# Optimization experiments

Hardware: AMD Instinct MI355X
Metric: run time of the kernel (lower is better)

Reference implementation:

```python
import jax, jax.numpy as jnp
import numpy as np

N, E, F = 50000, 800000, 16  # nodes, edges, per-quaternion-component features


def setup_inputs() -> dict:
    key = jax.random.key(0)
    ks = jax.random.split(key, 6)
    q = jax.random.normal(ks[0], (4, N, F), jnp.float32)          # node quaternion feats (r,i,j,k)
    edge_attr = jax.random.normal(ks[1], (4, E, F), jnp.float32)  # edge quaternion feats
    edge_index = jax.random.randint(ks[2], (2, E), 0, N)          # [src; dst]
    W1 = jax.random.normal(ks[3], (4, F, F), jnp.float32) * 0.1   # QLinear 1 weights (r,i,j,k)
    b1 = jnp.zeros((4, F), jnp.float32)
    W2 = jax.random.normal(ks[4], (4, F, F), jnp.float32) * 0.1   # QLinear 2 weights
    b2 = jnp.zeros((4, F), jnp.float32)
    beta = jnp.ones((1,), jnp.float32)                            # softmax temperature
    return {"q": q, "edge_attr": edge_attr, "edge_index": edge_index,
            "W1": W1, "b1": b1, "W2": W2, "b2": b2, "beta": beta}


def _qlinear(x, W, b):
    # Quaternion (Hamilton) linear: x [4,M,F_in], W [4,F_in,F_out], b [4,F_out]
    xr, xi, xj, xk = x
    Wr, Wi, Wj, Wk = W
    r = xr @ Wr - xi @ Wi - xj @ Wj - xk @ Wk
    i = xr @ Wi + xi @ Wr + xj @ Wk - xk @ Wj
    j = xr @ Wj - xi @ Wk + xj @ Wr + xk @ Wi
    k = xr @ Wk + xi @ Wj - xj @ Wi + xk @ Wr
    return jnp.stack([r, i, j, k]) + b[:, None, :]


def reference(q, edge_attr, edge_index, W1, b1, W2, b2, beta):
    src, dst = edge_index[0], edge_index[1]
    # message: gather source features, add edge attrs (identity msg_encoder)
    msg = q[:, src, :] + edge_attr                      # [4,E,F]
    m2 = msg.transpose(1, 0, 2).reshape(E, 4 * F)       # stacked layout, as in forward()
    # segment (per-dst-node) softmax over edges, elementwise per feature
    z = m2 * beta[0]
    zmax = jax.ops.segment_max(z, dst, num_segments=N)  # [N,4F]
    ez = jnp.exp(z - zmax[dst])
    denom = jax.ops.segment_sum(ez, dst, num_segments=N)
    alpha = ez / denom[dst]                             # scatter_softmax weights
    agg = jax.ops.segment_sum(m2 * alpha, dst, num_segments=N)  # [N,4F]
    agg = agg.reshape(N, 4, F).transpose(1, 0, 2)       # back to [4,N,F]
    # self-loop residual then 2-layer quaternion MLP (relu, no norm)
    x = q + agg
    h = jax.nn.relu(_qlinear(x, W1, b1))
    return _qlinear(h, W2, b2)
```

## Files before the change

### kernel.cpp

```cpp
#include <hip/hip_runtime.h>
#include <hip/hip_fp16.h>


#define FDIM 16
#define CF 64
#define CAP 64

typedef _Float16 f16x8 __attribute__((ext_vector_type(8)));
typedef float f32x4 __attribute__((ext_vector_type(4)));

__global__ __launch_bounds__(256) void k_init(
    int* __restrict__ cursor, const float* __restrict__ W1,
    const float* __restrict__ W2, _Float16* __restrict__ wfrag,
    const float* __restrict__ q, _Float16* __restrict__ qT,
    int N, int zb) {
  int b = blockIdx.x;
  if (b < zb) {
    int t = b * 256 + threadIdx.x;
    if (t < N) cursor[t] = 0;
  } else if (b < zb + 32) {
    int idx = (b - zb) * 256 + threadIdx.x;
    if (idx >= 8192) return;
    int jj = idx & 7;
    int l  = (idx >> 3) & 63;
    int ks = (idx >> 9) & 1;
    int t  = (idx >> 10) & 3;
    int L  = (idx >> 12) & 1;
    int k = ks * 32 + (l >> 4) * 8 + jj;
    int j = t * 16 + (l & 15);
    int ci = k >> 4, fi = k & 15, c = j >> 4, f = j & 15;
    float sgn = ((0x428Eu >> ((c << 2) | ci)) & 1u) ? -1.f : 1.f;
    const float* W = L ? W2 : W1;
    wfrag[idx] = (_Float16)(sgn * W[(((c ^ ci) * 16) + fi) * 16 + f]);
  } else {
    int t = (b - zb - 32) * 256 + threadIdx.x;
    int n = t >> 3;
    if (n >= N) return;
    int l8 = t & 7;
    int c = l8 >> 1, fh = (l8 & 1) * 8;
    const float4 a = *(const float4*)&q[((size_t)c * N + n) * FDIM + fh];
    const float4 bb = *(const float4*)&q[((size_t)c * N + n) * FDIM + fh + 4];
    f16x8 o;
    o[0]=(_Float16)a.x;  o[1]=(_Float16)a.y;  o[2]=(_Float16)a.z;  o[3]=(_Float16)a.w;
    o[4]=(_Float16)bb.x; o[5]=(_Float16)bb.y; o[6]=(_Float16)bb.z; o[7]=(_Float16)bb.w;
    *(f16x8*)(qT + (size_t)n * CF + l8 * 8) = o;
  }
}

__global__ __launch_bounds__(256) void k_permute(
    const _Float16* __restrict__ qT, const float* __restrict__ edge_attr,
    const int* __restrict__ edge_index, int* __restrict__ cursor,
    _Float16* __restrict__ rows, int N, int E) {
  int tid = threadIdx.x;
  int l = tid & 63;
  int wid = tid >> 6;
  int eg = l >> 3, l8 = l & 7;
  int c = l8 >> 1, fh = (l8 & 1) * 8;
  int e = blockIdx.x * 32 + wid * 8 + eg;
  bool valid = (e < E);
  int ec = valid ? e : 0;
  int src = 0, slot = 0, dst = 0;
  if (l8 == 0 && valid) {
    src = edge_index[ec];
    dst = edge_index[E + ec];
    slot = atomicAdd(&cursor[dst], 1);
  }
  src  = __shfl(src,  l & 56);
  slot = __shfl(slot, l & 56);
  dst  = __shfl(dst,  l & 56);
  if (!valid || slot >= CAP) return;
  const float* eap = &edge_attr[((size_t)c * E + ec) * FDIM + fh];
  f32x4 ea0 = __builtin_nontemporal_load((const f32x4*)eap);
  f32x4 ea1 = __builtin_nontemporal_load((const f32x4*)(eap + 4));
  const f16x8 qv = *(const f16x8*)(qT + (size_t)src * CF + l8 * 8);
  f16x8 o;
  o[0] = (_Float16)(ea0[0] + (float)qv[0]);
  o[1] = (_Float16)(ea0[1] + (float)qv[1]);
  o[2] = (_Float16)(ea0[2] + (float)qv[2]);
  o[3] = (_Float16)(ea0[3] + (float)qv[3]);
  o[4] = (_Float16)(ea1[0] + (float)qv[4]);
  o[5] = (_Float16)(ea1[1] + (float)qv[5]);
  o[6] = (_Float16)(ea1[2] + (float)qv[6]);
  o[7] = (_Float16)(ea1[3] + (float)qv[7]);
  __builtin_nontemporal_store(
      o, (f16x8*)(rows + ((size_t)dst * CAP + slot) * CF + l8 * 8));
}

__global__ __launch_bounds__(256) void k_reduce(
    const _Float16* __restrict__ qT,
    const _Float16* __restrict__ rows,
    const int* __restrict__ cursor,
    const float* __restrict__ beta_p,
    _Float16* __restrict__ xbuf, int N) {
  int tid = threadIdx.x;
  int wave = tid >> 6, l = tid & 63;
  int g = l >> 3, ch = l & 7;
  int n = blockIdx.x * 4 + wave;
  if (n >= N) return;
  float beta = beta_p[0];
  int cnt = min(cursor[n], CAP);
  size_t base = (size_t)n * CAP;

  float num0=0,num1=0,num2=0,num3=0,num4=0,num5=0,num6=0,num7=0;
  float den0=0,den1=0,den2=0,den3=0,den4=0,den5=0,den6=0,den7=0;
  for (int i = 0; i < cnt; i += 8) {
    int idx = i + g;
    bool v = (idx < cnt);
    const f16x8 u = __builtin_nontemporal_load(
        (const f16x8*)(rows + (base + (v ? idx : 0)) * CF + ch * 8));
    float msk = v ? 1.f : 0.f;
    float m0=(float)u[0], m1=(float)u[1], m2=(float)u[2], m3=(float)u[3];
    float m4=(float)u[4], m5=(float)u[5], m6=(float)u[6], m7=(float)u[7];
    float e0=__expf(m0*beta)*msk, e1=__expf(m1*beta)*msk;
    float e2=__expf(m2*beta)*msk, e3=__expf(m3*beta)*msk;
    float e4=__expf(m4*beta)*msk, e5=__expf(m5*beta)*msk;
    float e6=__expf(m6*beta)*msk, e7=__expf(m7*beta)*msk;
    den0+=e0; num0=fmaf(m0,e0,num0); den1+=e1; num1=fmaf(m1,e1,num1);
    den2+=e2; num2=fmaf(m2,e2,num2); den3+=e3; num3=fmaf(m3,e3,num3);
    den4+=e4; num4=fmaf(m4,e4,num4); den5+=e5; num5=fmaf(m5,e5,num5);
    den6+=e6; num6=fmaf(m6,e6,num6); den7+=e7; num7=fmaf(m7,e7,num7);
  }
  #pragma unroll
  for (int off = 8; off <= 32; off <<= 1) {
    num0 += __shfl_xor(num0, off); den0 += __shfl_xor(den0, off);
    num1 += __shfl_xor(num1, off); den1 += __shfl_xor(den1, off);
    num2 += __shfl_xor(num2, off); den2 += __shfl_xor(den2, off);
    num3 += __shfl_xor(num3, off); den3 += __shfl_xor(den3, off);
    num4 += __shfl_xor(num4, off); den4 += __shfl_xor(den4, off);
    num5 += __shfl_xor(num5, off); den5 += __shfl_xor(den5, off);
    num6 += __shfl_xor(num6, off); den6 += __shfl_xor(den6, off);
    num7 += __shfl_xor(num7, off); den7 += __shfl_xor(den7, off);
  }
  if (g == 0) {
    const f16x8 qv = *(const f16x8*)(qT + (size_t)n * CF + ch * 8);
    f16x8 xo;
    xo[0]=(_Float16)((float)qv[0] + (den0>0.f?num0/den0:0.f));
    xo[1]=(_Float16)((float)qv[1] + (den1>0.f?num1/den1:0.f));
    xo[2]=(_Float16)((float)qv[2] + (den2>0.f?num2/den2:0.f));
    xo[3]=(_Float16)((float)qv[3] + (den3>0.f?num3/den3:0.f));
    xo[4]=(_Float16)((float)qv[4] + (den4>0.f?num4/den4:0.f));
    xo[5]=(_Float16)((float)qv[5] + (den5>0.f?num5/den5:0.f));
    xo[6]=(_Float16)((float)qv[6] + (den6>0.f?num6/den6:0.f));
    xo[7]=(_Float16)((float)qv[7] + (den7>0.f?num7/den7:0.f));
    *(f16x8*)(xbuf + (size_t)n * CF + ch * 8) = xo;
  }
}

#define HL_STRIDE 72
__global__ __launch_bounds__(256) void k_mlp(
    const _Float16* __restrict__ xbuf,
    const _Float16* __restrict__ wfrag,
    const float* __restrict__ b1, const float* __restrict__ b2,
    float* __restrict__ out, int N) {
  __shared__ _Float16 hl[4][16][HL_STRIDE];
  int tid = threadIdx.x, wave = tid >> 6, l = tid & 63;
  int n0 = (blockIdx.x * 4 + wave) * 16;
  bool valid = (n0 < N);
  int nb = valid ? n0 : 0;
  int cl = l & 15, kg = l >> 4;

  const f16x8* wf = (const f16x8*)wfrag;
  f16x8 a0 = *(const f16x8*)(xbuf + ((size_t)(nb + cl)) * CF + kg * 8);
  f16x8 a1 = *(const f16x8*)(xbuf + ((size_t)(nb + cl)) * CF + 32 + kg * 8);

  f32x4 c0 = {0,0,0,0}, c1 = {0,0,0,0}, c2 = {0,0,0,0}, c3 = {0,0,0,0};
  c0 = __builtin_amdgcn_mfma_f32_16x16x32_f16(a0, wf[(0*2+0)*64+l], c0, 0,0,0);
  c0 = __builtin_amdgcn_mfma_f32_16x16x32_f16(a1, wf[(0*2+1)*64+l], c0, 0,0,0);
  c1 = __builtin_amdgcn_mfma_f32_16x16x32_f16(a0, wf[(1*2+0)*64+l], c1, 0,0,0);
  c1 = __builtin_amdgcn_mfma_f32_16x16x32_f16(a1, wf[(1*2+1)*64+l], c1, 0,0,0);
  c2 = __builtin_amdgcn_mfma_f32_16x16x32_f16(a0, wf[(2*2+0)*64+l], c2, 0,0,0);
  c2 = __builtin_amdgcn_mfma_f32_16x16x32_f16(a1, wf[(2*2+1)*64+l], c2, 0,0,0);
  c3 = __builtin_amdgcn_mfma_f32_16x16x32_f16(a0, wf[(3*2+0)*64+l], c3, 0,0,0);
  c3 = __builtin_amdgcn_mfma_f32_16x16x32_f16(a1, wf[(3*2+1)*64+l], c3, 0,0,0);

  float bb0 = b1[0*16+cl], bb1 = b1[1*16+cl], bb2 = b1[2*16+cl], bb3 = b1[3*16+cl];
  #pragma unroll
  for (int r = 0; r < 4; ++r) {
    int row = kg * 4 + r;
    hl[wave][row][0*16+cl] = (_Float16)fmaxf(c0[r] + bb0, 0.f);
    hl[wave][row][1*16+cl] = (_Float16)fmaxf(c1[r] + bb1, 0.f);
    hl[wave][row][2*16+cl] = (_Float16)fmaxf(c2[r] + bb2, 0.f);
    hl[wave][row][3*16+cl] = (_Float16)fmaxf(c3[r] + bb3, 0.f);
  }
  __syncthreads();

  f16x8 h0 = *(const f16x8*)&hl[wave][cl][kg * 8];
  f16x8 h1 = *(const f16x8*)&hl[wave][cl][32 + kg * 8];

  f32x4 d0 = {0,0,0,0}, d1 = {0,0,0,0}, d2 = {0,0,0,0}, d3 = {0,0,0,0};
  d0 = __builtin_amdgcn_mfma_f32_16x16x32_f16(h0, wf[(8+0*2+0)*64+l], d0, 0,0,0);
  d0 = __builtin_amdgcn_mfma_f32_16x16x32_f16(h1, wf[(8+0*2+1)*64+l], d0, 0,0,0);
  d1 = __builtin_amdgcn_mfma_f32_16x16x32_f16(h0, wf[(8+1*2+0)*64+l], d1, 0,0,0);
  d1 = __builtin_amdgcn_mfma_f32_16x16x32_f16(h1, wf[(8+1*2+1)*64+l], d1, 0,0,0);
  d2 = __builtin_amdgcn_mfma_f32_16x16x32_f16(h0, wf[(8+2*2+0)*64+l], d2, 0,0,0);
  d2 = __builtin_amdgcn_mfma_f32_16x16x32_f16(h1, wf[(8+2*2+1)*64+l], d2, 0,0,0);
  d3 = __builtin_amdgcn_mfma_f32_16x16x32_f16(h0, wf[(8+3*2+0)*64+l], d3, 0,0,0);
  d3 = __builtin_amdgcn_mfma_f32_16x16x32_f16(h1, wf[(8+3*2+1)*64+l], d3, 0,0,0);

  if (valid) {
    float cb0 = b2[0*16+cl], cb1 = b2[1*16+cl], cb2 = b2[2*16+cl], cb3 = b2[3*16+cl];
    #pragma unroll
    for (int r = 0; r < 4; ++r) {
      int n = n0 + kg * 4 + r;
      out[((size_t)0 * N + n) * FDIM + cl] = d0[r] + cb0;
      out[((size_t)1 * N + n) * FDIM + cl] = d1[r] + cb1;
      out[((size_t)2 * N + n) * FDIM + cl] = d2[r] + cb2;
      out[((size_t)3 * N + n) * FDIM + cl] = d3[r] + cb3;
    }
  }
}

__global__ __launch_bounds__(256) void k_zero(int* __restrict__ p, int n) {
  int t = blockIdx.x * 256 + threadIdx.x;
  if (t < n) p[t] = 0;
}

__global__ __launch_bounds__(256) void k_hist(const int* __restrict__ edge_index,
                                              int* __restrict__ counts, int E) {
  int e = blockIdx.x * 256 + threadIdx.x;
  if (e >= E) return;
  atomicAdd(&counts[edge_index[E + e]], 1);
}

__global__ __launch_bounds__(1024) void k_scan_fb(int* __restrict__ counts,
                                                  int* __restrict__ node_start,
                                                  int N, int E) {
  __shared__ int part[1024];
  int t = threadIdx.x;
  int seg = (N + 1023) / 1024;
  int base = t * seg;
  int lim = min(base + seg, N);
  int s = 0;
  for (int i = base; i < lim; ++i) s += counts[i];
  part[t] = s;
  __syncthreads();
  for (int off = 1; off < 1024; off <<= 1) {
    int v = (t >= off) ? part[t - off] : 0;
    __syncthreads();
    part[t] += v;
    __syncthreads();
  }
  int run = part[t] - s;
  for (int i = base; i < lim; ++i) {
    int c = counts[i];
    node_start[i] = run;
    counts[i] = run;
    run += c;
  }
  if (t == 1023) node_start[N] = E;
}

__global__ __launch_bounds__(256) void k_scatter2(const int* __restrict__ edge_index,
                                                  int* __restrict__ cursor,
                                                  int2* __restrict__ sorted, int E) {
  int e = blockIdx.x * 256 + threadIdx.x;
  if (e >= E) return;
  int src = edge_index[e];
  int dst = edge_index[E + e];
  int pos = atomicAdd(&cursor[dst], 1);
  sorted[pos] = make_int2(e, src);
}

__global__ __launch_bounds__(256) void k_node(
    const float* __restrict__ q, const float* __restrict__ edge_attr,
    const int2* __restrict__ sorted, const int* __restrict__ node_start,
    const float* __restrict__ beta_p,
    const float* __restrict__ W1, const float* __restrict__ b1,
    const float* __restrict__ W2, const float* __restrict__ b2,
    float* __restrict__ out, int N, int E) {
  __shared__ float w1s[1024], w2s[1024], b1s[64], b2s[64];
  __shared__ float xs[4][64], hs[4][64];
  int tid = threadIdx.x;
  for (int i = tid; i < 1024; i += 256) { w1s[i] = W1[i]; w2s[i] = W2[i]; }
  if (tid < 64) { b1s[tid] = b1[tid]; b2s[tid] = b2[tid]; }
  int wave = tid >> 6, l = tid & 63, c = l >> 4, f = l & 15;
  int n = blockIdx.x * 4 + wave;
  float beta = beta_p[0];
  float x = 0.f;
  if (n < N) {
    int start = node_start[n], end = node_start[n + 1];
    float den = 0.f, num = 0.f;
    for (int i = start; i < end; ++i) {
      int2 es = sorted[i];
      float qa = q[((size_t)c * N + es.y) * FDIM + f];
      float ea = edge_attr[((size_t)c * E + es.x) * FDIM + f];
      float m2 = qa + ea;
      float ez = __expf(m2 * beta);
      den += ez;
      num = fmaf(m2, ez, num);
    }
    float agg = (den > 0.f) ? num / den : 0.f;
    x = q[((size_t)c * N + n) * FDIM + f] + agg;
  }
  xs[wave][l] = x;
  __syncthreads();
  const unsigned negmask = 0x428Eu;
  float acc = b1s[l];
  #pragma unroll
  for (int ci = 0; ci < 4; ++ci) {
    int wc = c ^ ci;
    float s = ((negmask >> ((c << 2) | ci)) & 1u) ? -1.f : 1.f;
    #pragma unroll
    for (int fi = 0; fi < FDIM; ++fi)
      acc = fmaf(s * xs[wave][ci * FDIM + fi], w1s[wc * 256 + fi * FDIM + f], acc);
  }
  hs[wave][l] = fmaxf(acc, 0.f);
  __syncthreads();
  float acc2 = b2s[l];
  #pragma unroll
  for (int ci = 0; ci < 4; ++ci) {
    int wc = c ^ ci;
    float s = ((negmask >> ((c << 2) | ci)) & 1u) ? -1.f : 1.f;
    #pragma unroll
    for (int fi = 0; fi < FDIM; ++fi)
      acc2 = fmaf(s * hs[wave][ci * FDIM + fi], w2s[wc * 256 + fi * FDIM + f], acc2);
  }
  if (n < N) out[((size_t)c * N + n) * FDIM + f] = acc2;
}

extern "C" void kernel_launch(void* const* d_in, const int* in_sizes, int n_in,
                              void* d_out, int out_size, void* d_ws, size_t ws_size,
                              hipStream_t stream) {
  const float* q         = (const float*)d_in[0];
  const float* edge_attr = (const float*)d_in[1];
  const int*   edge_idx  = (const int*)d_in[2];
  const float* W1        = (const float*)d_in[3];
  const float* b1        = (const float*)d_in[4];
  const float* W2        = (const float*)d_in[5];
  const float* b2        = (const float*)d_in[6];
  const float* beta      = (const float*)d_in[7];

  int N = in_sizes[0] / CF;
  int E = in_sizes[2] / 2;

  int* cursor = (int*)d_ws;
  size_t off_w = ((size_t)N * sizeof(int) + 255) & ~(size_t)255;
  _Float16* wfrag = (_Float16*)((char*)d_ws + off_w);
  size_t off_q = off_w + 8192 * sizeof(_Float16);
  _Float16* qT = (_Float16*)((char*)d_ws + off_q);
  size_t off_x = off_q + (size_t)N * CF * sizeof(_Float16);
  _Float16* xbuf = (_Float16*)((char*)d_ws + off_x);
  size_t off_r = (off_x + (size_t)N * CF * sizeof(_Float16) + 255) & ~(size_t)255;
  _Float16* rows = (_Float16*)((char*)d_ws + off_r);
  size_t needed = off_r + (size_t)N * CAP * CF * sizeof(_Float16);

  if (ws_size >= needed && (N % 16) == 0) {
    int zb = (N + 255) / 256;
    int qb = (N * 8 + 255) / 256;
    k_init<<<zb + 32 + qb, 256, 0, stream>>>(cursor, W1, W2, wfrag, q, qT, N, zb);
    k_permute<<<(E + 31) / 32, 256, 0, stream>>>(qT, edge_attr, edge_idx,
                                                 cursor, rows, N, E);
    k_reduce<<<(N + 3) / 4, 256, 0, stream>>>(qT, rows, cursor, beta, xbuf, N);
    k_mlp<<<(N / 16 + 3) / 4, 256, 0, stream>>>(xbuf, wfrag, b1, b2,
                                                (float*)d_out, N);
  } else {
    int* counts     = (int*)d_ws;
    int* node_start = counts + N;
    size_t off8 = ((size_t)(2 * N + 1) * sizeof(int) + 7) & ~(size_t)7;
    int2* sorted2 = (int2*)((char*)d_ws + off8);
    int eblocks = (E + 255) / 256;
    k_zero<<<(N + 255) / 256, 256, 0, stream>>>(counts, N);
    k_hist<<<eblocks, 256, 0, stream>>>(edge_idx, counts, E);
    k_scan_fb<<<1, 1024, 0, stream>>>(counts, node_start, N, E);
    k_scatter2<<<eblocks, 256, 0, stream>>>(edge_idx, counts, sorted2, E);
    k_node<<<(N + 3) / 4, 256, 0, stream>>>(q, edge_attr, sorted2, node_start,
                                            beta, W1, b1, W2, b2,
                                            (float*)d_out, N, E);
  }
}
```

Baseline: 136.3 us.

## Fuse segment-softmax reduce into quaternion MLP kernel and shrink slot capacity

Measured after the change: 153.7 us. 12.8% more time.

```diff
diff --git a/kernel.cpp b/kernel.cpp
--- a/kernel.cpp
+++ b/kernel.cpp
@@ -4,7 +4,7 @@
 
 #define FDIM 16
 #define CF 64
-#define CAP 64
+#define CAP 48
 
 typedef _Float16 f16x8 __attribute__((ext_vector_type(8)));
 typedef float f32x4 __attribute__((ext_vector_type(4)));
@@ -86,82 +86,82 @@
       o, (f16x8*)(rows + ((size_t)dst * CAP + slot) * CF + l8 * 8));
 }
 
-__global__ __launch_bounds__(256) void k_reduce(
+#define XW_STRIDE 72
+__global__ __launch_bounds__(256) void k_redmlp(
     const _Float16* __restrict__ qT,
     const _Float16* __restrict__ rows,
     const int* __restrict__ cursor,
     const float* __restrict__ beta_p,
-    _Float16* __restrict__ xbuf, int N) {
-  int tid = threadIdx.x;
-  int wave = tid >> 6, l = tid & 63;
-  int g = l >> 3, ch = l & 7;
-  int n = blockIdx.x * 4 + wave;
-  if (n >= N) return;
-  float beta = beta_p[0];
-  int cnt = min(cursor[n], CAP);
-  size_t base = (size_t)n * CAP;
-
-  float num0=0,num1=0,num2=0,num3=0,num4=0,num5=0,num6=0,num7=0;
-  float den0=0,den1=0,den2=0,den3=0,den4=0,den5=0,den6=0,den7=0;
-  for (int i = 0; i < cnt; i += 8) {
-    int idx = i + g;
-    bool v = (idx < cnt);
-    const f16x8 u = __builtin_nontemporal_load(
-        (const f16x8*)(rows + (base + (v ? idx : 0)) * CF + ch * 8));
-    float msk = v ? 1.f : 0.f;
-    float m0=(float)u[0], m1=(float)u[1], m2=(float)u[2], m3=(float)u[3];
-    float m4=(float)u[4], m5=(float)u[5], m6=(float)u[6], m7=(float)u[7];
-    float e0=__expf(m0*beta)*msk, e1=__expf(m1*beta)*msk;
-    float e2=__expf(m2*beta)*msk, e3=__expf(m3*beta)*msk;
-    float e4=__expf(m4*beta)*msk, e5=__expf(m5*beta)*msk;
-    float e6=__expf(m6*beta)*msk, e7=__expf(m7*beta)*msk;
-    den0+=e0; num0=fmaf(m0,e0,num0); den1+=e1; num1=fmaf(m1,e1,num1);
-    den2+=e2; num2=fmaf(m2,e2,num2); den3+=e3; num3=fmaf(m3,e3,num3);
-    den4+=e4; num4=fmaf(m4,e4,num4); den5+=e5; num5=fmaf(m5,e5,num5);
-    den6+=e6; num6=fmaf(m6,e6,num6); den7+=e7; num7=fmaf(m7,e7,num7);
-  }
-  #pragma unroll
-  for (int off = 8; off <= 32; off <<= 1) {
-    num0 += __shfl_xor(num0, off); den0 += __shfl_xor(den0, off);
-    num1 += __shfl_xor(num1, off); den1 += __shfl_xor(den1, off);
-    num2 += __shfl_xor(num2, off); den2 += __shfl_xor(den2, off);
-    num3 += __shfl_xor(num3, off); den3 += __shfl_xor(den3, off);
-    num4 += __shfl_xor(num4, off); den4 += __shfl_xor(den4, off);
-    num5 += __shfl_xor(num5, off); den5 += __shfl_xor(den5, off);
-    num6 += __shfl_xor(num6, off); den6 += __shfl_xor(den6, off);
-    num7 += __shfl_xor(num7, off); den7 += __shfl_xor(den7, off);
-  }
-  if (g == 0) {
-    const f16x8 qv = *(const f16x8*)(qT + (size_t)n * CF + ch * 8);
-    f16x8 xo;
-    xo[0]=(_Float16)((float)qv[0] + (den0>0.f?num0/den0:0.f));
-    xo[1]=(_Float16)((float)qv[1] + (den1>0.f?num1/den1:0.f));
-    xo[2]=(_Float16)((float)qv[2] + (den2>0.f?num2/den2:0.f));
-    xo[3]=(_Float16)((float)qv[3] + (den3>0.f?num3/den3:0.f));
-    xo[4]=(_Float16)((float)qv[4] + (den4>0.f?num4/den4:0.f));
-    xo[5]=(_Float16)((float)qv[5] + (den5>0.f?num5/den5:0.f));
-    xo[6]=(_Float16)((float)qv[6] + (den6>0.f?num6/den6:0.f));
-    xo[7]=(_Float16)((float)qv[7] + (den7>0.f?num7/den7:0.f));
-    *(f16x8*)(xbuf + (size_t)n * CF + ch * 8) = xo;
-  }
-}
-
-#define HL_STRIDE 72
-__global__ __launch_bounds__(256) void k_mlp(
-    const _Float16* __restrict__ xbuf,
     const _Float16* __restrict__ wfrag,
     const float* __restrict__ b1, const float* __restrict__ b2,
     float* __restrict__ out, int N) {
-  __shared__ _Float16 hl[4][16][HL_STRIDE];
+  __shared__ _Float16 xw[4][16][XW_STRIDE];
+  __shared__ _Float16 hl[4][16][XW_STRIDE];
   int tid = threadIdx.x, wave = tid >> 6, l = tid & 63;
+  int g = l >> 3, ch = l & 7;
   int n0 = (blockIdx.x * 4 + wave) * 16;
-  bool valid = (n0 < N);
-  int nb = valid ? n0 : 0;
+  float beta = beta_p[0];
+
+  for (int j = 0; j < 16; ++j) {
+    int n = n0 + j;
+    bool nv = (n < N);
+    float num0=0,num1=0,num2=0,num3=0,num4=0,num5=0,num6=0,num7=0;
+    float den0=0,den1=0,den2=0,den3=0,den4=0,den5=0,den6=0,den7=0;
+    if (nv) {
+      int cnt = min(cursor[n], CAP);
+      size_t base = (size_t)n * CAP;
+      for (int i = 0; i < cnt; i += 8) {
+        int idx = i + g;
+        bool v = (idx < cnt);
+        const f16x8 u = __builtin_nontemporal_load(
+            (const f16x8*)(rows + (base + (v ? idx : 0)) * CF + ch * 8));
+        float msk = v ? 1.f : 0.f;
+        float m0=(float)u[0], m1=(float)u[1], m2=(float)u[2], m3=(float)u[3];
+        float m4=(float)u[4], m5=(float)u[5], m6=(float)u[6], m7=(float)u[7];
+        float e0=__expf(m0*beta)*msk, e1=__expf(m1*beta)*msk;
+        float e2=__expf(m2*beta)*msk, e3=__expf(m3*beta)*msk;
+        float e4=__expf(m4*beta)*msk, e5=__expf(m5*beta)*msk;
+        float e6=__expf(m6*beta)*msk, e7=__expf(m7*beta)*msk;
+        den0+=e0; num0=fmaf(m0,e0,num0); den1+=e1; num1=fmaf(m1,e1,num1);
+        den2+=e2; num2=fmaf(m2,e2,num2); den3+=e3; num3=fmaf(m3,e3,num3);
+        den4+=e4; num4=fmaf(m4,e4,num4); den5+=e5; num5=fmaf(m5,e5,num5);
+        den6+=e6; num6=fmaf(m6,e6,num6); den7+=e7; num7=fmaf(m7,e7,num7);
+      }
+    }
+    #pragma unroll
+    for (int off = 8; off <= 32; off <<= 1) {
+      num0 += __shfl_xor(num0, off); den0 += __shfl_xor(den0, off);
+      num1 += __shfl_xor(num1, off); den1 += __shfl_xor(den1, off);
+      num2 += __shfl_xor(num2, off); den2 += __shfl_xor(den2, off);
+      num3 += __shfl_xor(num3, off); den3 += __shfl_xor(den3, off);
+      num4 += __shfl_xor(num4, off); den4 += __shfl_xor(den4, off);
+      num5 += __shfl_xor(num5, off); den5 += __shfl_xor(den5, off);
+      num6 += __shfl_xor(num6, off); den6 += __shfl_xor(den6, off);
+      num7 += __shfl_xor(num7, off); den7 += __shfl_xor(den7, off);
+    }
+    if (g == 0) {
+      f16x8 xo;
+      if (nv) {
+        const f16x8 qv = *(const f16x8*)(qT + (size_t)n * CF + ch * 8);
+        xo[0]=(_Float16)((float)qv[0] + (den0>0.f?num0/den0:0.f));
+        xo[1]=(_Float16)((float)qv[1] + (den1>0.f?num1/den1:0.f));
+        xo[2]=(_Float16)((float)qv[2] + (den2>0.f?num2/den2:0.f));
+        xo[3]=(_Float16)((float)qv[3] + (den3>0.f?num3/den3:0.f));
+        xo[4]=(_Float16)((float)qv[4] + (den4>0.f?num4/den4:0.f));
+        xo[5]=(_Float16)((float)qv[5] + (den5>0.f?num5/den5:0.f));
+        xo[6]=(_Float16)((float)qv[6] + (den6>0.f?num6/den6:0.f));
+        xo[7]=(_Float16)((float)qv[7] + (den7>0.f?num7/den7:0.f));
+      } else {
+        xo = (f16x8)(_Float16)0.f;
+      }
+      *(f16x8*)&xw[wave][j][ch * 8] = xo;
+    }
+  }
+
   int cl = l & 15, kg = l >> 4;
-
   const f16x8* wf = (const f16x8*)wfrag;
-  f16x8 a0 = *(const f16x8*)(xbuf + ((size_t)(nb + cl)) * CF + kg * 8);
-  f16x8 a1 = *(const f16x8*)(xbuf + ((size_t)(nb + cl)) * CF + 32 + kg * 8);
+  f16x8 a0 = *(const f16x8*)&xw[wave][cl][kg * 8];
+  f16x8 a1 = *(const f16x8*)&xw[wave][cl][32 + kg * 8];
 
   f32x4 c0 = {0,0,0,0}, c1 = {0,0,0,0}, c2 = {0,0,0,0}, c3 = {0,0,0,0};
   c0 = __builtin_amdgcn_mfma_f32_16x16x32_f16(a0, wf[(0*2+0)*64+l], c0, 0,0,0);
@@ -182,7 +182,6 @@
     hl[wave][row][2*16+cl] = (_Float16)fmaxf(c2[r] + bb2, 0.f);
     hl[wave][row][3*16+cl] = (_Float16)fmaxf(c3[r] + bb3, 0.f);
   }
-  __syncthreads();
 
   f16x8 h0 = *(const f16x8*)&hl[wave][cl][kg * 8];
   f16x8 h1 = *(const f16x8*)&hl[wave][cl][32 + kg * 8];
@@ -197,11 +196,11 @@
   d3 = __builtin_amdgcn_mfma_f32_16x16x32_f16(h0, wf[(8+3*2+0)*64+l], d3, 0,0,0);
   d3 = __builtin_amdgcn_mfma_f32_16x16x32_f16(h1, wf[(8+3*2+1)*64+l], d3, 0,0,0);
 
-  if (valid) {
-    float cb0 = b2[0*16+cl], cb1 = b2[1*16+cl], cb2 = b2[2*16+cl], cb3 = b2[3*16+cl];
-    #pragma unroll
-    for (int r = 0; r < 4; ++r) {
-      int n = n0 + kg * 4 + r;
+  float cb0 = b2[0*16+cl], cb1 = b2[1*16+cl], cb2 = b2[2*16+cl], cb3 = b2[3*16+cl];
+  #pragma unroll
+  for (int r = 0; r < 4; ++r) {
+    int n = n0 + kg * 4 + r;
+    if (n < N) {
       out[((size_t)0 * N + n) * FDIM + cl] = d0[r] + cb0;
       out[((size_t)1 * N + n) * FDIM + cl] = d1[r] + cb1;
       out[((size_t)2 * N + n) * FDIM + cl] = d2[r] + cb2;
@@ -338,9 +337,7 @@
   _Float16* wfrag = (_Float16*)((char*)d_ws + off_w);
   size_t off_q = off_w + 8192 * sizeof(_Float16);
   _Float16* qT = (_Float16*)((char*)d_ws + off_q);
-  size_t off_x = off_q + (size_t)N * CF * sizeof(_Float16);
-  _Float16* xbuf = (_Float16*)((char*)d_ws + off_x);
-  size_t off_r = (off_x + (size_t)N * CF * sizeof(_Float16) + 255) & ~(size_t)255;
+  size_t off_r = (off_q + (size_t)N * CF * sizeof(_Float16) + 255) & ~(size_t)255;
   _Float16* rows = (_Float16*)((char*)d_ws + off_r);
   size_t needed = off_r + (size_t)N * CAP * CF * sizeof(_Float16);
 
@@ -350,9 +347,9 @@
     k_init<<<zb + 32 + qb, 256, 0, stream>>>(cursor, W1, W2, wfrag, q, qT, N, zb);
     k_permute<<<(E + 31) / 32, 256, 0, stream>>>(qT, edge_attr, edge_idx,
                                                  cursor, rows, N, E);
-    k_reduce<<<(N + 3) / 4, 256, 0, stream>>>(qT, rows, cursor, beta, xbuf, N);
-    k_mlp<<<(N / 16 + 3) / 4, 256, 0, stream>>>(xbuf, wfrag, b1, b2,
-                                                (float*)d_out, N);
+    int nwb = (N + 63) / 64;
+    k_redmlp<<<nwb, 256, 0, stream>>>(qT, rows, cursor, beta, wfrag,
+                                      b1, b2, (float*)d_out, N);
   } else {
     int* counts     = (int*)d_ws;
     int* node_start = counts + N;
```
